# Optimization experiments

Hardware: AMD Instinct MI355X
Metric: run time of the kernel (lower is better)

The kernel has to match this reference:

```python
import jax, jax.numpy as jnp
import numpy as np

B, D, F, T, H = 256, 128, 8, 128, 128


def setup_inputs() -> dict:
    key = jax.random.key(0)
    ks = jax.random.split(key, 6)
    inp = jax.random.normal(ks[0], (B, D, F, T), jnp.float32)
    # encode_attn: Linear(F*T + 2*H -> 1); weight laid out as [hidden | cell | x]
    w_attn = jax.random.normal(ks[1], (F * T + 2 * H,), jnp.float32) * 0.02
    b_attn = jax.random.normal(ks[2], (), jnp.float32) * 0.02
    # LSTM (single layer), PyTorch gate order i, f, g, o
    W_ih = jax.random.normal(ks[3], (4 * H, D * F), jnp.float32) * 0.02
    W_hh = jax.random.normal(ks[4], (4 * H, H), jnp.float32) * 0.02
    b_ih = jax.random.normal(ks[5], (4 * H,), jnp.float32) * 0.02
    b_hh = jnp.zeros((4 * H,), jnp.float32)
    return {"input": inp, "w_attn": w_attn, "b_attn": b_attn,
            "W_ih": W_ih, "W_hh": W_hh, "b_ih": b_ih, "b_hh": b_hh}


def reference(input, w_attn, b_attn, W_ih, W_hh, b_ih, b_hh):
    Bd, Dd, Fd, Td = input.shape
    Hd = W_hh.shape[1]
    # split attention weight per cat order: (hidden_state, cell_state, x)
    w_h = w_attn[:Hd]
    w_c = w_attn[Hd:2 * Hd]
    w_x = w_attn[2 * Hd:]
    x_flat = input.reshape(Bd, Dd, Fd * Td)           # [B, D, F*T]
    ex = x_flat @ w_x                                  # [B, D], constant over t
    xs = jnp.moveaxis(input, 3, 0)                     # [T, B, D, F]

    def step(carry, x_t):
        h, c = carry                                   # [B, H] each
        # attention logits: h/c contributions are per-batch scalars broadcast over drives
        e = ex + (h @ w_h + c @ w_c + b_attn)[:, None]  # [B, D]
        a = jax.nn.softmax(e, axis=-1)                 # softmax over drives
        x_hat = (a[:, :, None] * x_t).reshape(Bd, Dd * Fd)  # [B, D*F]
        gates = x_hat @ W_ih.T + h @ W_hh.T + b_ih + b_hh   # [B, 4H]
        i, f, g, o = jnp.split(gates, 4, axis=-1)
        c_new = jax.nn.sigmoid(f) * c + jax.nn.sigmoid(i) * jnp.tanh(g)
        h_new = jax.nn.sigmoid(o) * jnp.tanh(c_new)
        return (h_new, c_new), h_new

    h0 = jnp.zeros((Bd, Hd), input.dtype)
    c0 = jnp.zeros((Bd, Hd), input.dtype)
    _, hs = jax.lax.scan(step, (h0, c0), xs)           # hs: [T, B, H]
    return jnp.transpose(hs, (1, 0, 2))                # [B, T, H] == hidden_states[:, 1:]
```

## Files before the change

### kernel.cpp

```cpp
#include <hip/hip_runtime.h>
#include <cstdint>
#include <cstddef>

#define Bn 256
#define Dn 128
#define Fn 8
#define Tn 128
#define Hn 128
#define Kn 1024
#define Mn 512

typedef float f32x4 __attribute__((ext_vector_type(4)));
typedef short s16x8 __attribute__((ext_vector_type(8)));
typedef _Float16 h16x2 __attribute__((ext_vector_type(2)));
typedef _Float16 h16x8 __attribute__((ext_vector_type(8)));

#if defined(__has_builtin)
#if __has_builtin(__builtin_amdgcn_fdot2)
#define HAVE_FDOT2 1
#else
#define HAVE_FDOT2 0
#endif
#if __has_builtin(__builtin_amdgcn_cvt_pkrtz)
#define HAVE_PKRTZ 1
#else
#define HAVE_PKRTZ 0
#endif
#else
#define HAVE_FDOT2 0
#define HAVE_PKRTZ 0
#endif

__device__ __forceinline__ uint32_t pack2_f16(float a, float b) {
#if HAVE_PKRTZ
  typedef __fp16 fp16x2_t __attribute__((ext_vector_type(2)));
  union { fp16x2_t v; uint32_t u; } cv;
  cv.v = __builtin_amdgcn_cvt_pkrtz(a, b);
  return cv.u;
#else
  union { h16x2 h; uint32_t u; } cv;
  cv.h.x = (_Float16)a; cv.h.y = (_Float16)b;
  return cv.u;
#endif
}
__device__ __forceinline__ float sigm(float x) { return 1.0f / (1.0f + __expf(-x)); }
__device__ __forceinline__ float tanh_fast(float x) { return 1.0f - 2.0f / (__expf(2.0f * x) + 1.0f); }

__global__ __launch_bounds__(256) void k_ex(const float* __restrict__ input,
                                            const float* __restrict__ w_attn,
                                            float* __restrict__ ex) {
  __shared__ float wx[Kn];
  const int tid = threadIdx.x;
  ((float4*)wx)[tid] = ((const float4*)(w_attn + 2 * Hn))[tid];
  __syncthreads();
  const int w = tid >> 6, lane = tid & 63;
  const int gid = blockIdx.x * 4 + w;
  const float4* xp = (const float4*)(input + (size_t)gid * Kn);
  const float4* wx4 = (const float4*)wx;
  float acc = 0.f;
#pragma unroll
  for (int r = 0; r < 4; ++r) {
    float4 x = xp[lane + r * 64];
    float4 ww = wx4[lane + r * 64];
    acc += x.x * ww.x + x.y * ww.y + x.z * ww.z + x.w * ww.w;
  }
#pragma unroll
  for (int off = 32; off; off >>= 1) acc += __shfl_xor(acc, off);
  if (lane == 0) ex[gid] = acc;
}

__global__ __launch_bounds__(256) void k_prep(const float* __restrict__ W_ih,
                                              const float* __restrict__ W_hh,
                                              unsigned short* __restrict__ whf,
                                              uint32_t* __restrict__ whhp) {
  const int bid = blockIdx.x;
  const int tid = threadIdx.x;
  if (bid < 256) {
    const int gid = bid * 256 + tid;
    const int lane = gid & 63;
    const int kt = (gid >> 6) & 31;
    const int mt = gid >> 11;
    const int row = mt * 16 + (lane & 15);
    const int col = kt * 32 + (lane >> 4) * 8;
    const float* src = W_ih + row * Kn + col;
    uint4 ph;
    ph.x = pack2_f16(src[0], src[1]);
    ph.y = pack2_f16(src[2], src[3]);
    ph.z = pack2_f16(src[4], src[5]);
    ph.w = pack2_f16(src[6], src[7]);
    ((uint4*)whf)[gid] = ph;
  } else {
    const int g = (bid - 256) * 256 + tid;
    const int j = g & 511, kk = g >> 9;
    float2 wv = ((const float2*)(W_hh + (size_t)j * Hn))[kk];
    h16x2 t2; t2.x = (_Float16)wv.x; t2.y = (_Float16)wv.y;
    union { h16x2 h; uint32_t u; } cv; cv.h = t2;
    whhp[kk * 512 + j] = cv.u;
  }
}

__global__ __launch_bounds__(256, 2) void k_gates(
    const float* __restrict__ input, const float* __restrict__ ex,
    const unsigned short* __restrict__ whf,
    unsigned short* __restrict__ gx) {
  __shared__ __align__(16) unsigned char smem[34816];
  __shared__ float a_lds[Dn];
  __shared__ float sred[8];
  unsigned short* buf0 = (unsigned short*)smem;
  unsigned short* buf1 = buf0 + 8192;
  _Float16* lds_out = (_Float16*)smem;

  const int tid = threadIdx.x;
  const int bid = blockIdx.x;
  const int p = (bid >> 3) & 3;
  const int b = (bid & 7) | ((bid >> 5) << 3);
  const int w = tid >> 6;
  const int lane = tid & 63;
  const int quad = lane >> 4;
  const int l15 = lane & 15;

  float v = (tid < Dn) ? ex[b * Dn + tid] : -3.4e38f;
  float m = v;
#pragma unroll
  for (int off = 32; off; off >>= 1) m = fmaxf(m, __shfl_xor(m, off));
  if (lane == 0) sred[w] = m;
  __syncthreads();
  m = fmaxf(fmaxf(sred[0], sred[1]), fmaxf(sred[2], sred[3]));
  float e = (tid < Dn) ? __expf(v - m) : 0.f;
  float s = e;
#pragma unroll
  for (int off = 32; off; off >>= 1) s += __shfl_xor(s, off);
  if (lane == 0) sred[4 + w] = s;
  __syncthreads();
  s = sred[4] + sred[5] + sred[6] + sred[7];
  if (tid < Dn) a_lds[tid] = e / s;

  f32x4 acc[2][8];
#pragma unroll
  for (int i = 0; i < 2; ++i)
#pragma unroll
    for (int j = 0; j < 8; ++j) { f32x4 z = {0.f, 0.f, 0.f, 0.f}; acc[i][j] = z; }

  const float* xb = input + (size_t)b * Kn * Tn;
  const int mtg0 = p * 8 + w * 2;

  h16x8 wcur[4], wnxt[4];
#pragma unroll
  for (int mt = 0; mt < 2; ++mt)
#pragma unroll
    for (int kf = 0; kf < 2; ++kf) {
      const size_t fo = (((size_t)(mtg0 + mt) * 32 + kf) * 64 + lane) * 8;
      wcur[mt * 2 + kf] = *(const h16x8*)(whf + fo);
    }

  __syncthreads();

  float xr[2][2][8];
#pragma unroll
  for (int ck = 0; ck < 2; ++ck)
#pragma unroll
    for (int ct = 0; ct < 2; ++ct) {
      const int kb = 2 * w + ck;
      const float* col = xb + (size_t)(kb * 8) * Tn + lane + 64 * ct;
#pragma unroll
      for (int j = 0; j < 8; ++j) xr[ck][ct][j] = col[(size_t)j * Tn];
    }
#pragma unroll
  for (int ck = 0; ck < 2; ++ck) {
    const int kb = 2 * w + ck;
    const float av = a_lds[kb];
#pragma unroll
    for (int ct = 0; ct < 2; ++ct) {
      const int tt = lane + 64 * ct;
      uint4 pk;
      pk.x = pack2_f16(av * xr[ck][ct][0], av * xr[ck][ct][1]);
      pk.y = pack2_f16(av * xr[ck][ct][2], av * xr[ck][ct][3]);
      pk.z = pack2_f16(av * xr[ck][ct][4], av * xr[ck][ct][5]);
      pk.w = pack2_f16(av * xr[ck][ct][6], av * xr[ck][ct][7]);
      *(uint4*)(buf0 + (size_t)(kb * 128 + tt) * 8) = pk;
    }
  }
  __syncthreads();

  for (int kt = 0; kt < 16; ++kt) {
    unsigned short* cur = (kt & 1) ? buf1 : buf0;
    unsigned short* nxt = (kt & 1) ? buf0 : buf1;
    if (kt < 15) {
      const int k0n = (kt + 1) * 64;
#pragma unroll
      for (int ck = 0; ck < 2; ++ck)
#pragma unroll
        for (int ct = 0; ct < 2; ++ct) {
          const int kb = 2 * w + ck;
          const float* col = xb + (size_t)(k0n + kb * 8) * Tn + lane + 64 * ct;
#pragma unroll
          for (int j = 0; j < 8; ++j) xr[ck][ct][j] = col[(size_t)j * Tn];
        }
#pragma unroll
      for (int mt = 0; mt < 2; ++mt)
#pragma unroll
        for (int kf = 0; kf < 2; ++kf) {
          const size_t fo = (((size_t)(mtg0 + mt) * 32 + (kt + 1) * 2 + kf) * 64 + lane) * 8;
          wnxt[mt * 2 + kf] = *(const h16x8*)(whf + fo);
        }
    }
#pragma unroll
    for (int kf = 0; kf < 2; ++kf) {
      h16x8 bfr[8];
      const int kbr = kf * 4 + quad;
#pragma unroll
      for (int nt = 0; nt < 8; ++nt)
        bfr[nt] = *(const h16x8*)(cur + (size_t)(kbr * 128 + nt * 16 + l15) * 8);
#pragma unroll
      for (int mt = 0; mt < 2; ++mt)
#pragma unroll
        for (int nt = 0; nt < 8; ++nt) {
          acc[mt][nt] = __builtin_amdgcn_mfma_f32_16x16x32_f16(wcur[mt * 2 + kf], bfr[nt], acc[mt][nt], 0, 0, 0);
        }
    }
    if (kt < 15) {
#pragma unroll
      for (int ck = 0; ck < 2; ++ck) {
        const int kb = 2 * w + ck;
        const float av = a_lds[(kt + 1) * 8 + kb];
#pragma unroll
        for (int ct = 0; ct < 2; ++ct) {
          const int tt = lane + 64 * ct;
          uint4 pk;
          pk.x = pack2_f16(av * xr[ck][ct][0], av * xr[ck][ct][1]);
          pk.y = pack2_f16(av * xr[ck][ct][2], av * xr[ck][ct][3]);
          pk.z = pack2_f16(av * xr[ck][ct][4], av * xr[ck][ct][5]);
          pk.w = pack2_f16(av * xr[ck][ct][6], av * xr[ck][ct][7]);
          *(uint4*)(nxt + (size_t)(kb * 128 + tt) * 8) = pk;
        }
      }
#pragma unroll
      for (int i = 0; i < 4; ++i) wcur[i] = wnxt[i];
    }
    __syncthreads();
  }

#pragma unroll
  for (int mt = 0; mt < 2; ++mt)
#pragma unroll
    for (int nt = 0; nt < 8; ++nt)
#pragma unroll
      for (int r = 0; r < 4; ++r) {
        const int jl = (w * 2 + mt) * 16 + quad * 4 + r;
        lds_out[jl * 136 + nt * 16 + l15] = (_Float16)acc[mt][nt][r];
      }
  __syncthreads();
  {
    const int jr = tid >> 1, half = tid & 1;
    const uint4* lsrc = (const uint4*)(lds_out + jr * 136 + half * 64);
    uint4* gdst = (uint4*)(gx + ((size_t)(b * Mn + p * 128 + jr)) * Tn + half * 64);
#pragma unroll
    for (int i = 0; i < 8; ++i) gdst[i] = lsrc[i];
  }
}

__global__ __launch_bounds__(256) void k_rec(
    const unsigned short* __restrict__ gx, const uint32_t* __restrict__ whhp,
    const float* __restrict__ b_ih, const float* __restrict__ b_hh,
    float* __restrict__ out) {
  __shared__ unsigned short gxl[512 * 130];
  __shared__ float gstep[Mn];
  __shared__ __align__(16) _Float16 h2l[Hn];

  const int tid = threadIdx.x;
  const int b = blockIdx.x;

  {
    const uint4* src = (const uint4*)(gx + (size_t)b * Mn * Tn);
#pragma unroll
    for (int it = 0; it < 32; ++it) {
      const int c = it * 256 + tid;
      const int row = c >> 4, off = c & 15;
      uint4 vv = src[c];
      uint32_t* dst = (uint32_t*)((char*)gxl + (size_t)row * 260 + off * 16);
      dst[0] = vv.x; dst[1] = vv.y; dst[2] = vv.z; dst[3] = vv.w;
    }
  }
  const int j0 = tid, j1 = tid + 256;
  const float bs0 = b_ih[j0] + b_hh[j0];
  const float bs1 = b_ih[j1] + b_hh[j1];
  h16x2 wr0[64], wr1[64];
#pragma unroll
  for (int kk = 0; kk < 64; ++kk) {
    union { uint32_t u; h16x2 h; } c0, c1;
    c0.u = whhp[kk * 512 + j0];
    c1.u = whhp[kk * 512 + j1];
    wr0[kk] = c0.h; wr1[kk] = c1.h;
  }
  if (tid < Hn) h2l[tid] = (_Float16)0.f;
  float c_st = 0.f;
  __syncthreads();

  float* outp = out + (size_t)b * Tn * Hn;
  for (int t = 0; t < Tn; ++t) {
    float g0 = bs0 + (float)(*(const _Float16*)&gxl[j0 * 130 + t]);
    float g1 = bs1 + (float)(*(const _Float16*)&gxl[j1 * 130 + t]);
    float a0 = 0.f, a1 = 0.f, a2 = 0.f, a3 = 0.f;
    float d0 = 0.f, d1 = 0.f, d2 = 0.f, d3 = 0.f;
    const h16x8* hv = (const h16x8*)h2l;
#pragma unroll
    for (int q = 0; q < 16; ++q) {
      union { h16x8 v; h16x2 pr[4]; } u; u.v = hv[q];
#if HAVE_FDOT2
      a0 = __builtin_amdgcn_fdot2(wr0[q * 4 + 0], u.pr[0], a0, false);
      a1 = __builtin_amdgcn_fdot2(wr0[q * 4 + 1], u.pr[1], a1, false);
      a2 = __builtin_amdgcn_fdot2(wr0[q * 4 + 2], u.pr[2], a2, false);
      a3 = __builtin_amdgcn_fdot2(wr0[q * 4 + 3], u.pr[3], a3, false);
      d0 = __builtin_amdgcn_fdot2(wr1[q * 4 + 0], u.pr[0], d0, false);
      d1 = __builtin_amdgcn_fdot2(wr1[q * 4 + 1], u.pr[1], d1, false);
      d2 = __builtin_amdgcn_fdot2(wr1[q * 4 + 2], u.pr[2], d2, false);
      d3 = __builtin_amdgcn_fdot2(wr1[q * 4 + 3], u.pr[3], d3, false);
#else
#pragma unroll
      for (int z = 0; z < 4; ++z) {
        a0 += (float)wr0[q * 4 + z].x * (float)u.pr[z].x + (float)wr0[q * 4 + z].y * (float)u.pr[z].y;
        d0 += (float)wr1[q * 4 + z].x * (float)u.pr[z].x + (float)wr1[q * 4 + z].y * (float)u.pr[z].y;
      }
#endif
    }
    gstep[j0] = (a0 + a1) + (a2 + a3) + g0;
    gstep[j1] = (d0 + d1) + (d2 + d3) + g1;
    __syncthreads();
    const int d = tid & 127;
    const float gi = gstep[d];
    const float gf = gstep[Hn + d];
    const float gg = gstep[2 * Hn + d];
    const float go = gstep[3 * Hn + d];
    c_st = sigm(gf) * c_st + sigm(gi) * tanh_fast(gg);
    const float hnew = sigm(go) * tanh_fast(c_st);
    if (tid < Hn) {
      outp[t * Hn + d] = hnew;
      h2l[d] = (_Float16)hnew;
    }
    __syncthreads();
  }
}

extern "C" void kernel_launch(void* const* d_in, const int* in_sizes, int n_in,
                              void* d_out, int out_size, void* d_ws, size_t ws_size,
                              hipStream_t stream) {
  (void)in_sizes; (void)n_in; (void)out_size; (void)ws_size;
  const float* input = (const float*)d_in[0];
  const float* w_attn = (const float*)d_in[1];
  const float* W_ih = (const float*)d_in[3];
  const float* W_hh = (const float*)d_in[4];
  const float* b_ih = (const float*)d_in[5];
  const float* b_hh = (const float*)d_in[6];
  float* out = (float*)d_out;

  char* ws = (char*)d_ws;
  float* ex = (float*)ws;
  unsigned short* whf = (unsigned short*)(ws + 131072);
  uint32_t* whhp = (uint32_t*)(ws + 1179648);
  unsigned short* gxw = (unsigned short*)(ws + 1310720);

  k_ex<<<8192, 256, 0, stream>>>(input, w_attn, ex);
  k_prep<<<384, 256, 0, stream>>>(W_ih, W_hh, whf, whhp);
  k_gates<<<1024, 256, 0, stream>>>(input, ex, whf, gxw);
  k_rec<<<Bn, 256, 0, stream>>>(gxw, whhp, b_ih, b_hh, out);
}
```

Baseline: 359.1 us.

## Exchange LSTM gates via wave shuffles and double-buffer hidden state to drop a barrier

Remaps the recurrent kernel's gate rows so that each wavefront's lanes hold the i/f/g/o gates for the same hidden unit, split across the two 32-lane halves. The gates are then exchanged with __shfl_xor instead of going through a shared gstep array. The hidden-state buffer is double-buffered by timestep parity, so one of the two __syncthreads per step can be removed. The aim is to shorten the serial per-timestep critical path, at the cost of shuffle instructions and a more intricate index mapping.

```diff
diff --git a/kernel.cpp b/kernel.cpp
--- a/kernel.cpp
+++ b/kernel.cpp
@@ -264,8 +264,7 @@
     const float* __restrict__ b_ih, const float* __restrict__ b_hh,
     float* __restrict__ out) {
   __shared__ unsigned short gxl[512 * 130];
-  __shared__ float gstep[Mn];
-  __shared__ __align__(16) _Float16 h2l[Hn];
+  __shared__ __align__(16) _Float16 h2l[2][Hn];
 
   const int tid = threadIdx.x;
   const int b = blockIdx.x;
@@ -281,7 +280,11 @@
       dst[0] = vv.x; dst[1] = vv.y; dst[2] = vv.z; dst[3] = vv.w;
     }
   }
-  const int j0 = tid, j1 = tid + 256;
+  const int w = tid >> 6, l = tid & 63;
+  const bool lo = (l < 32);
+  const int d = w * 32 + (l & 31);
+  const int j0 = d + (lo ? 0 : 128);
+  const int j1 = j0 + 256;
   const float bs0 = b_ih[j0] + b_hh[j0];
   const float bs1 = b_ih[j1] + b_hh[j1];
   h16x2 wr0[64], wr1[64];
@@ -292,7 +295,7 @@
     c1.u = whhp[kk * 512 + j1];
     wr0[kk] = c0.h; wr1[kk] = c1.h;
   }
-  if (tid < Hn) h2l[tid] = (_Float16)0.f;
+  if (tid < Hn) h2l[0][tid] = (_Float16)0.f;
   float c_st = 0.f;
   __syncthreads();
 
@@ -302,7 +305,7 @@
     float g1 = bs1 + (float)(*(const _Float16*)&gxl[j1 * 130 + t]);
     float a0 = 0.f, a1 = 0.f, a2 = 0.f, a3 = 0.f;
     float d0 = 0.f, d1 = 0.f, d2 = 0.f, d3 = 0.f;
-    const h16x8* hv = (const h16x8*)h2l;
+    const h16x8* hv = (const h16x8*)(&h2l[t & 1][0]);
 #pragma unroll
     for (int q = 0; q < 16; ++q) {
       union { h16x8 v; h16x2 pr[4]; } u; u.v = hv[q];
@@ -323,19 +326,19 @@
       }
 #endif
     }
-    gstep[j0] = (a0 + a1) + (a2 + a3) + g0;
-    gstep[j1] = (d0 + d1) + (d2 + d3) + g1;
-    __syncthreads();
-    const int d = tid & 127;
-    const float gi = gstep[d];
-    const float gf = gstep[Hn + d];
-    const float gg = gstep[2 * Hn + d];
-    const float go = gstep[3 * Hn + d];
+    const float a = (a0 + a1) + (a2 + a3) + g0;
+    const float bb = (d0 + d1) + (d2 + d3) + g1;
+    const float aX = __shfl_xor(a, 32);
+    const float bX = __shfl_xor(bb, 32);
+    const float gi = lo ? a : aX;
+    const float gf = lo ? aX : a;
+    const float gg = lo ? bb : bX;
+    const float go = lo ? bX : bb;
     c_st = sigm(gf) * c_st + sigm(gi) * tanh_fast(gg);
     const float hnew = sigm(go) * tanh_fast(c_st);
-    if (tid < Hn) {
+    if (lo) {
       outp[t * Hn + d] = hnew;
-      h2l[d] = (_Float16)hnew;
+      h2l[(t + 1) & 1][d] = (_Float16)hnew;
     }
     __syncthreads();
   }
```

New measurement: 357.2 us. No clear change (-0.5%).
